# Performance work log

Measured on AMD Instinct MI355X. Metric: run time of the kernel, lower is better.

## Reference

```python
import jax, jax.numpy as jnp
import numpy as np
from jax import lax

E = 300   # word embedding dim (hard-coded embedding_size in DMCNN)
P = 5     # position-feature dim
H = 200   # conv out channels
S = 256   # max_seq_len
L = 34    # num_labels
VOCAB = 21128


def setup_inputs() -> dict:
    key = jax.random.key(0)
    ks = jax.random.split(key, 7)
    B = 8
    return {
        "inputs": jax.random.randint(ks[0], (B, S), 0, VOCAB, dtype=jnp.int64),
        "word_emb": jax.random.normal(ks[1], (VOCAB, E), dtype=jnp.float32) * 0.02,
        "pf_emb": jax.random.normal(ks[2], (S, P), dtype=jnp.float32) * 0.02,
        "conv_W": jax.random.normal(ks[3], (H, E + P, 3), dtype=jnp.float32) * 0.02,
        "conv_b": jax.random.normal(ks[4], (H,), dtype=jnp.float32) * 0.02,
        "fc_W": jax.random.normal(ks[5], (L, 3 * E + 2 * H), dtype=jnp.float32) * 0.02,
        "fc_b": jax.random.normal(ks[6], (L,), dtype=jnp.float32) * 0.02,
    }


def _conv1d(x_ncs, w_oik):
    # x: [N, C, S], w: [O, I, K], stride 1, padding 1 (kernel 3)
    return lax.conv_general_dilated(
        x_ncs, w_oik, window_strides=(1,), padding=[(1, 1)],
        dimension_numbers=("NCH", "OIH", "NCH"))


def reference(inputs, word_emb, pf_emb, conv_W, conv_b, fc_W, fc_b):
    B = inputs.shape[0]
    tok = word_emb[inputs]                       # [B, S, E]

    # Positions i = 1 .. S-2 (the original loop), fully vectorized.
    i_vals = jnp.arange(1, S - 1)                # [S-2]
    j = jnp.arange(S)
    pos_idx = jnp.abs(j[None, :] - i_vals[:, None])   # [S-2, S] == the loop's pos_index
    pf = pf_emb[pos_idx]                         # [S-2, S, P]

    # Conv is linear: split into token part (shared across i) + pf part (per i).
    W_tok, W_pf = conv_W[:, :E, :], conv_W[:, E:, :]
    conv_tok = _conv1d(tok.transpose(0, 2, 1), W_tok) + conv_b[None, :, None]  # [B, H, S]
    conv_pf = _conv1d(pf.transpose(0, 2, 1), W_pf)                             # [S-2, H, S] (batch-independent)

    out = jax.nn.relu(conv_tok[None] + conv_pf[:, None])   # [S-2, B, H, S]

    # Dynamic split max-pool at index i.
    left_mask = (j[None, :] < i_vals[:, None])[:, None, None, :]  # [S-2,1,1,S]
    neg_inf = jnp.array(-jnp.inf, dtype=out.dtype)
    max_left = jnp.where(left_mask, out, neg_inf).max(axis=-1)    # [S-2, B, H]
    max_right = jnp.where(left_mask, neg_inf, out).max(axis=-1)   # [S-2, B, H]
    pool = jnp.concatenate([max_left, max_right], axis=-1)        # [S-2, B, 2H]

    # Lexical-level features: window [i-1, i, i+1] flattened.
    llf = jnp.concatenate([tok[:, 0:S - 2], tok[:, 1:S - 1], tok[:, 2:S]], axis=-1)  # [B, S-2, 3E]

    feat = jnp.concatenate([pool.transpose(1, 0, 2), llf], axis=-1)  # [B, S-2, 2H+3E]
    logits_mid = jnp.einsum("bsf,lf->bsl", feat, fc_W) + fc_b        # [B, S-2, L]

    pad = jnp.zeros((B, 1, L), dtype=logits_mid.dtype).at[:, :, -1].set(1.0)
    return jnp.concatenate([pad, logits_mid, pad], axis=1)          # [B, S, L]
```

## Files before the change

kernel.cpp:

```cpp
#include <hip/hip_runtime.h>

#define E 300
#define P 5
#define H 200
#define S 256
#define L 34
#define B 8
#define NI 254

typedef __attribute__((ext_vector_type(8))) short short8;
typedef __attribute__((ext_vector_type(4))) float f32x4;

#define TOKB_OFF   0
#define TOKB_FL    309632
#define WR3_OFF    (TOKB_OFF+TOKB_FL)
#define WR3_FL     96512
#define FCWB_OFF   (WR3_OFF+WR3_FL)
#define FCWB_FL    32256
#define G_OFF      (FCWB_OFF+FCWB_FL)
#define G_FL       102400
#define C0_OFF     (G_OFF+G_FL)
#define C0_FL      50800
#define C255_OFF   (C0_OFF+C0_FL)
#define C255_FL    50800
#define CT_OFF     (C255_OFF+C255_FL)
#define CT_FL      409600
#define POOLBF_OFF (CT_OFF+CT_FL)
#define POOLBF_FL  425984

__device__ __forceinline__ unsigned short f2bf(float f) {
    unsigned u = __float_as_uint(f);
    unsigned r = (u + 0x7FFFu + ((u >> 16) & 1u)) >> 16;
    return (unsigned short)r;
}
__device__ __forceinline__ short8 load_a8(const unsigned short* p) {
    short8 r;
    ((ushort4*)&r)[0] = *(const ushort4*)p;
    ((ushort4*)&r)[1] = *(const ushort4*)(p + 4);
    return r;
}
__device__ __forceinline__ float4 add4(float4 a, float4 b) {
    return make_float4(a.x+b.x, a.y+b.y, a.z+b.z, a.w+b.w);
}
__device__ __forceinline__ float4 max4(float4 a, float4 b) {
    return make_float4(fmaxf(a.x,b.x), fmaxf(a.y,b.y), fmaxf(a.z,b.z), fmaxf(a.w,b.w));
}

#define GA_BLOCKS 605
#define PREP_BLOCKS 1803

__global__ __launch_bounds__(256) void k_init(const int* __restrict__ ids,
                                              const float* __restrict__ we,
                                              const float* __restrict__ convW,
                                              const float* __restrict__ fcW,
                                              const float* __restrict__ pf,
                                              unsigned short* __restrict__ tokb,
                                              unsigned short* __restrict__ Wr3,
                                              unsigned short* __restrict__ fcWb,
                                              float* __restrict__ g,
                                              float* __restrict__ c0,
                                              float* __restrict__ c255) {
    if (blockIdx.x < GA_BLOCKS) {
        int idx = blockIdx.x * 256 + threadIdx.x;
        const int total = B * 258 * 75;
        if (idx >= total) return;
        int row = idx / 75;
        int col = idx - row * 75;
        int b = row / 258;
        int r = row - b * 258;
        float4 v = make_float4(0.f, 0.f, 0.f, 0.f);
        if (r >= 1 && r <= 256) {
            int id = ids[b * S + (r - 1)];
            v = ((const float4*)we)[(size_t)id * 75 + col];
        }
        ushort4 o;
        o.x = f2bf(v.x); o.y = f2bf(v.y); o.z = f2bf(v.z); o.w = f2bf(v.w);
        *(ushort4*)(tokb + (size_t)row * 300 + col * 4) = o;
        return;
    }
    int idx = (blockIdx.x - GA_BLOCKS) * 256 + threadIdx.x;
    if (idx < 193024) {
        int hh = idx / 928, kk = idx - hh * 928;
        float v = 0.f;
        if (hh < H && kk < 900) {
            int r = kk / 300, e = kk - r * 300;
            v = convW[hh * 915 + e * 3 + r];
        }
        Wr3[idx] = f2bf(v);
    } else if (idx < 257536) {
        int t = idx - 193024;
        int l = t / 1344, c = t - l * 1344;
        float v = 0.f;
        if (l < L) {
            if (c < 400) v = fcW[l * 1300 + c];
            else if (c >= 416 && c < 1316) v = fcW[l * 1300 + 400 + (c - 416)];
        }
        fcWb[t] = f2bf(v);
    } else if (idx < 359936) {
        int t = idx - 257536;
        int t2 = t / H, h = t - t2 * H;
        int d = t2 - 256;
        float a = 0.f;
#pragma unroll
        for (int k = 0; k < 3; k++) {
            int r = d + k - 1; r = (r < 0) ? -r : r; if (r > 255) r = 255;
#pragma unroll
            for (int q = 0; q < P; q++)
                a += convW[h * 915 + (E + q) * 3 + k] * pf[r * P + q];
        }
        g[t] = a;
    } else if (idx < 410736) {
        int t = idx - 359936;
        int m = t / H, h = t - m * H;
        int i = m + 1;
        float a = 0.f;
#pragma unroll
        for (int q = 0; q < P; q++) {
            a += convW[h * 915 + (E + q) * 3 + 1] * pf[i * P + q];
            a += convW[h * 915 + (E + q) * 3 + 2] * pf[(i - 1) * P + q];
        }
        c0[m * H + h] = a;
    } else if (idx < 461536) {
        int t = idx - 410736;
        int m = t / H, h = t - m * H;
        int i = m + 1;
        float a = 0.f;
#pragma unroll
        for (int q = 0; q < P; q++) {
            a += convW[h * 915 + (E + q) * 3 + 0] * pf[(254 - i) * P + q];
            a += convW[h * 915 + (E + q) * 3 + 1] * pf[(255 - i) * P + q];
        }
        c255[m * H + h] = a;
    }
}

__global__ __launch_bounds__(256) void k_conv(const unsigned short* __restrict__ tokb,
                                              const unsigned short* __restrict__ Wr3,
                                              const float* __restrict__ convB,
                                              float* __restrict__ ct) {
    int n0 = blockIdx.x * 16;
    int mg = blockIdx.y;
    int wave = threadIdx.x >> 6;
    int lane = threadIdx.x & 63;
    int quad = lane >> 4;
    int lr = lane & 15;
    int mtile = mg * 4 + wave;
    int b = mtile >> 4;
    int j0 = (mtile & 15) << 4;

    const unsigned short* pa = tokb + ((size_t)(b * 258 + j0 + lr) * 300 + quad * 8);
    const unsigned short* pb = Wr3 + ((size_t)(n0 + lr) * 928 + quad * 8);

    f32x4 acc0 = {0.f, 0.f, 0.f, 0.f};
    f32x4 acc1 = {0.f, 0.f, 0.f, 0.f};
#pragma unroll
    for (int kk = 0; kk + 1 < 29; kk += 2) {
        short8 a0 = load_a8(pa + kk * 32);
        short8 b0 = *(const short8*)(pb + kk * 32);
        acc0 = __builtin_amdgcn_mfma_f32_16x16x32_bf16(a0, b0, acc0, 0, 0, 0);
        short8 a1 = load_a8(pa + kk * 32 + 32);
        short8 b1 = *(const short8*)(pb + kk * 32 + 32);
        acc1 = __builtin_amdgcn_mfma_f32_16x16x32_bf16(a1, b1, acc1, 0, 0, 0);
    }
    {
        short8 a0 = load_a8(pa + 28 * 32);
        short8 b0 = *(const short8*)(pb + 28 * 32);
        acc0 = __builtin_amdgcn_mfma_f32_16x16x32_bf16(a0, b0, acc0, 0, 0, 0);
    }
    int h = n0 + lr;
    if (h < H) {
        float bias = convB[h];
        float* cp = ct + ((size_t)(b * 256 + j0 + quad * 4) * 200 + h);
#pragma unroll
        for (int r = 0; r < 4; r++)
            cp[(size_t)r * 200] = acc0[r] + acc1[r] + bias;
    }
}

__global__ __launch_bounds__(512) void k_poolA(const float* __restrict__ ct,
                                               const float* __restrict__ g,
                                               const float* __restrict__ c0,
                                               const float* __restrict__ c255,
                                               unsigned short* __restrict__ poolbf) {
    __shared__ float4 lds4[8 * 4 * 2 * 50];
    int pg = blockIdx.x;
    int b  = blockIdx.y;
    int tid = threadIdx.x;
    int sub = tid >> 6;
    int lane = tid & 63;
    int p0 = pg * 4 + 1;

    if (lane < 50) {
        int h = lane << 2;
        const float* ctb = ct + (size_t)b * S * H + h;
        const float* gb  = g + h;

        float4 aL0 = {0,0,0,0}, aL1 = aL0, aL2 = aL0, aL3 = aL0;
        float4 aR0 = aL0, aR1 = aL0, aR2 = aL0, aR3 = aL0;

        if (sub == 0) {
            float4 c = *(const float4*)(ctb);
            int m = pg * 4;
            if (m + 0 < NI) aL0 = max4(aL0, add4(c, *(const float4*)(c0 + (m+0) * H + h)));
            if (m + 1 < NI) aL1 = max4(aL1, add4(c, *(const float4*)(c0 + (m+1) * H + h)));
            if (m + 2 < NI) aL2 = max4(aL2, add4(c, *(const float4*)(c0 + (m+2) * H + h)));
            if (m + 3 < NI) aL3 = max4(aL3, add4(c, *(const float4*)(c0 + (m+3) * H + h)));
        }
        if (sub == 7) {
            float4 c = *(const float4*)(ctb + (size_t)255 * H);
            int m = pg * 4;
            if (m + 0 < NI) aR0 = max4(aR0, add4(c, *(const float4*)(c255 + (m+0) * H + h)));
            if (m + 1 < NI) aR1 = max4(aR1, add4(c, *(const float4*)(c255 + (m+1) * H + h)));
            if (m + 2 < NI) aR2 = max4(aR2, add4(c, *(const float4*)(c255 + (m+2) * H + h)));
            if (m + 3 < NI) aR3 = max4(aR3, add4(c, *(const float4*)(c255 + (m+3) * H + h)));
        }

        int js = (sub == 0) ? 1 : sub * 32;
        int je = (sub == 7) ? 254 : sub * 32 + 31;

        float4 gr0 = *(const float4*)(gb + (size_t)(js - p0 + 256) * H);
        float4 gr1 = *(const float4*)(gb + (size_t)(js - p0 + 255) * H);
        float4 gr2 = *(const float4*)(gb + (size_t)(js - p0 + 254) * H);
        float4 gr3 = *(const float4*)(gb + (size_t)(js - p0 + 253) * H);

#pragma unroll 4
        for (int j = js; j <= je; ++j) {
            float4 c = *(const float4*)(ctb + (size_t)j * H);
            float4 v0 = add4(c, gr0);
            float4 v1 = add4(c, gr1);
            float4 v2 = add4(c, gr2);
            float4 v3 = add4(c, gr3);
            if (j < p0)     aL0 = max4(aL0, v0); else aR0 = max4(aR0, v0);
            if (j < p0 + 1) aL1 = max4(aL1, v1); else aR1 = max4(aR1, v1);
            if (j < p0 + 2) aL2 = max4(aL2, v2); else aR2 = max4(aR2, v2);
            if (j < p0 + 3) aL3 = max4(aL3, v3); else aR3 = max4(aR3, v3);
            gr3 = gr2; gr2 = gr1; gr1 = gr0;
            gr0 = *(const float4*)(gb + (size_t)(j + 1 - p0 + 256) * H);
        }

        float4* lp = lds4 + (size_t)sub * 400 + lane;
        lp[0]   = aL0; lp[50]  = aR0;
        lp[100] = aL1; lp[150] = aR1;
        lp[200] = aL2; lp[250] = aR2;
        lp[300] = aL3; lp[350] = aR3;
    }
    __syncthreads();

    if (tid < 400) {
        int k = tid / 100;
        int r = tid - k * 100;
        int half = r / 50;
        int ln = r - half * 50;
        int slot = (k * 2 + half) * 50 + ln;
        float4 v = lds4[slot];
#pragma unroll
        for (int s2 = 1; s2 < 8; s2++) v = max4(v, lds4[s2 * 400 + slot]);
        int m = pg * 4 + k;
        if (m < NI) {
            ushort4 o;
            o.x = f2bf(v.x); o.y = f2bf(v.y); o.z = f2bf(v.z); o.w = f2bf(v.w);
            *(ushort4*)(poolbf + (size_t)(b * 256 + m + 1) * 416 + half * 200 + ln * 4) = o;
        }
    } else if (tid < 464) {
        int t = tid - 400;
        int k = t >> 4, c = t & 15;
        int m = pg * 4 + k;
        if (m < NI) poolbf[(size_t)(b * 256 + m + 1) * 416 + 400 + c] = 0;
    }
}

__global__ __launch_bounds__(256) void k_fc(const unsigned short* __restrict__ poolbf,
                                            const unsigned short* __restrict__ tokb,
                                            const unsigned short* __restrict__ fcWb,
                                            const float* __restrict__ fcB,
                                            float* __restrict__ out) {
    int n0 = blockIdx.x * 16;
    int mg = blockIdx.y;
    int wave = threadIdx.x >> 6;
    int lane = threadIdx.x & 63;
    int quad = lane >> 4;
    int lr = lane & 15;
    int mtile = mg * 4 + wave;
    int b = mtile >> 4;
    int s0 = (mtile & 15) << 4;

    const unsigned short* pa0 = poolbf + ((size_t)(b * 256 + s0 + lr) * 416 + quad * 8);
    const unsigned short* pa1 = tokb + ((size_t)(b * 258 + s0 + lr) * 300 + quad * 8);
    const unsigned short* pb0 = fcWb + ((size_t)(n0 + lr) * 1344 + quad * 8);
    const unsigned short* pb1 = pb0 + 416;

    f32x4 acc0 = {0.f, 0.f, 0.f, 0.f};
    f32x4 acc1 = {0.f, 0.f, 0.f, 0.f};
    int kk = 0;
#pragma unroll 3
    for (kk = 0; kk + 1 < 13; kk += 2) {
        short8 a0 = load_a8(pa0 + kk * 32);
        short8 b0 = *(const short8*)(pb0 + kk * 32);
        acc0 = __builtin_amdgcn_mfma_f32_16x16x32_bf16(a0, b0, acc0, 0, 0, 0);
        short8 a1 = load_a8(pa0 + kk * 32 + 32);
        short8 b1 = *(const short8*)(pb0 + kk * 32 + 32);
        acc1 = __builtin_amdgcn_mfma_f32_16x16x32_bf16(a1, b1, acc1, 0, 0, 0);
    }
    {
        short8 a0 = load_a8(pa0 + 12 * 32);
        short8 b0 = *(const short8*)(pb0 + 12 * 32);
        acc0 = __builtin_amdgcn_mfma_f32_16x16x32_bf16(a0, b0, acc0, 0, 0, 0);
    }
#pragma unroll 4
    for (kk = 0; kk + 1 < 29; kk += 2) {
        short8 a0 = load_a8(pa1 + kk * 32);
        short8 b0 = *(const short8*)(pb1 + kk * 32);
        acc0 = __builtin_amdgcn_mfma_f32_16x16x32_bf16(a0, b0, acc0, 0, 0, 0);
        short8 a1 = load_a8(pa1 + kk * 32 + 32);
        short8 b1 = *(const short8*)(pb1 + kk * 32 + 32);
        acc1 = __builtin_amdgcn_mfma_f32_16x16x32_bf16(a1, b1, acc1, 0, 0, 0);
    }
    {
        short8 a0 = load_a8(pa1 + 28 * 32);
        short8 b0 = *(const short8*)(pb1 + 28 * 32);
        acc0 = __builtin_amdgcn_mfma_f32_16x16x32_bf16(a0, b0, acc0, 0, 0, 0);
    }

    int l = n0 + lr;
    if (l < L) {
        float bias = fcB[l];
#pragma unroll
        for (int r = 0; r < 4; r++) {
            int s = s0 + quad * 4 + r;
            float val;
            if (s == 0 || s == S - 1) val = (l == L - 1) ? 1.0f : 0.0f;
            else                      val = acc0[r] + acc1[r] + bias;
            out[(size_t)(b * 256 + s) * L + l] = val;
        }
    }
}

extern "C" void kernel_launch(void* const* d_in, const int* in_sizes, int n_in,
                              void* d_out, int out_size, void* d_ws, size_t ws_size,
                              hipStream_t stream) {
    const int*   ids      = (const int*)d_in[0];
    const float* word_emb = (const float*)d_in[1];
    const float* pf_emb   = (const float*)d_in[2];
    const float* conv_W   = (const float*)d_in[3];
    const float* conv_b   = (const float*)d_in[4];
    const float* fc_W     = (const float*)d_in[5];
    const float* fc_b     = (const float*)d_in[6];
    float* out = (float*)d_out;
    float* ws  = (float*)d_ws;

    unsigned short* tokb   = (unsigned short*)(ws + TOKB_OFF);
    unsigned short* Wr3    = (unsigned short*)(ws + WR3_OFF);
    unsigned short* fcWb   = (unsigned short*)(ws + FCWB_OFF);
    float* g     = ws + G_OFF;
    float* c0    = ws + C0_OFF;
    float* c255  = ws + C255_OFF;
    float* ct    = ws + CT_OFF;
    unsigned short* poolbf = (unsigned short*)(ws + POOLBF_OFF);

    k_init<<<GA_BLOCKS + PREP_BLOCKS, 256, 0, stream>>>(ids, word_emb, conv_W, fc_W,
                                                        pf_emb, tokb, Wr3, fcWb,
                                                        g, c0, c255);
    k_conv<<<dim3(13, 32), 256, 0, stream>>>(tokb, Wr3, conv_b, ct);
    k_poolA<<<dim3(64, 8), 512, 0, stream>>>(ct, g, c0, c255, poolbf);
    k_fc<<<dim3(3, 32), 256, 0, stream>>>(poolbf, tokb, fcWb, fc_b, out);
}
```

Before: 133.7 us.

## Store conv intermediates in bf16 and split pool loop into branch-free ranges

The conv output ct and the positional tables g, c0 and c255 are now stored as bf16 instead of fp32, which halves the bytes the pooling kernel reads from memory. The pooling j-loop is split into a pure-left range, a short mixed range of four iterations and a pure-right range, so the per-element left/right branch disappears from most iterations. The pool kernel also gets a min-blocks launch bound. The cost is lower precision in intermediates that feed a max, which could move outputs past tolerance.

```diff
diff --git a/kernel.cpp b/kernel.cpp
--- a/kernel.cpp
+++ b/kernel.cpp
@@ -13,25 +13,31 @@
 
 #define TOKB_OFF   0
 #define TOKB_FL    309632
-#define WR3_OFF    (TOKB_OFF+TOKB_FL)
+#define WR3_OFF    309632
 #define WR3_FL     96512
-#define FCWB_OFF   (WR3_OFF+WR3_FL)
+#define FCWB_OFF   406144
 #define FCWB_FL    32256
-#define G_OFF      (FCWB_OFF+FCWB_FL)
-#define G_FL       102400
-#define C0_OFF     (G_OFF+G_FL)
-#define C0_FL      50800
-#define C255_OFF   (C0_OFF+C0_FL)
-#define C255_FL    50800
-#define CT_OFF     (C255_OFF+C255_FL)
-#define CT_FL      409600
-#define POOLBF_OFF (CT_OFF+CT_FL)
+#define G_OFF      438400
+#define G_FL       51200
+#define C0_OFF     489600
+#define C0_FL      25400
+#define C255_OFF   515000
+#define C255_FL    25400
+#define CT_OFF     540400
+#define CT_FL      204800
+#define POOLBF_OFF 745200
 #define POOLBF_FL  425984
 
 __device__ __forceinline__ unsigned short f2bf(float f) {
     unsigned u = __float_as_uint(f);
     unsigned r = (u + 0x7FFFu + ((u >> 16) & 1u)) >> 16;
     return (unsigned short)r;
+}
+__device__ __forceinline__ float bfu(unsigned short s) {
+    return __uint_as_float(((unsigned)s) << 16);
+}
+__device__ __forceinline__ float4 bf4(ushort4 u) {
+    return make_float4(bfu(u.x), bfu(u.y), bfu(u.z), bfu(u.w));
 }
 __device__ __forceinline__ short8 load_a8(const unsigned short* p) {
     short8 r;
@@ -57,9 +63,9 @@
                                               unsigned short* __restrict__ tokb,
                                               unsigned short* __restrict__ Wr3,
                                               unsigned short* __restrict__ fcWb,
-                                              float* __restrict__ g,
-                                              float* __restrict__ c0,
-                                              float* __restrict__ c255) {
+                                              unsigned short* __restrict__ g,
+                                              unsigned short* __restrict__ c0,
+                                              unsigned short* __restrict__ c255) {
     if (blockIdx.x < GA_BLOCKS) {
         int idx = blockIdx.x * 256 + threadIdx.x;
         const int total = B * 258 * 75;
@@ -108,7 +114,7 @@
             for (int q = 0; q < P; q++)
                 a += convW[h * 915 + (E + q) * 3 + k] * pf[r * P + q];
         }
-        g[t] = a;
+        g[t] = f2bf(a);
     } else if (idx < 410736) {
         int t = idx - 359936;
         int m = t / H, h = t - m * H;
@@ -119,7 +125,7 @@
             a += convW[h * 915 + (E + q) * 3 + 1] * pf[i * P + q];
             a += convW[h * 915 + (E + q) * 3 + 2] * pf[(i - 1) * P + q];
         }
-        c0[m * H + h] = a;
+        c0[m * H + h] = f2bf(a);
     } else if (idx < 461536) {
         int t = idx - 410736;
         int m = t / H, h = t - m * H;
@@ -130,14 +136,14 @@
             a += convW[h * 915 + (E + q) * 3 + 0] * pf[(254 - i) * P + q];
             a += convW[h * 915 + (E + q) * 3 + 1] * pf[(255 - i) * P + q];
         }
-        c255[m * H + h] = a;
+        c255[m * H + h] = f2bf(a);
     }
 }
 
 __global__ __launch_bounds__(256) void k_conv(const unsigned short* __restrict__ tokb,
                                               const unsigned short* __restrict__ Wr3,
                                               const float* __restrict__ convB,
-                                              float* __restrict__ ct) {
+                                              unsigned short* __restrict__ ct) {
     int n0 = blockIdx.x * 16;
     int mg = blockIdx.y;
     int wave = threadIdx.x >> 6;
@@ -170,18 +176,17 @@
     int h = n0 + lr;
     if (h < H) {
         float bias = convB[h];
-        float* cp = ct + ((size_t)(b * 256 + j0 + quad * 4) * 200 + h);
 #pragma unroll
         for (int r = 0; r < 4; r++)
-            cp[(size_t)r * 200] = acc0[r] + acc1[r] + bias;
-    }
-}
-
-__global__ __launch_bounds__(512) void k_poolA(const float* __restrict__ ct,
-                                               const float* __restrict__ g,
-                                               const float* __restrict__ c0,
-                                               const float* __restrict__ c255,
-                                               unsigned short* __restrict__ poolbf) {
+            ct[(size_t)(b * 256 + j0 + quad * 4 + r) * 200 + h] = f2bf(acc0[r] + acc1[r] + bias);
+    }
+}
+
+__global__ __launch_bounds__(512, 4) void k_poolA(const unsigned short* __restrict__ ct,
+                                                  const unsigned short* __restrict__ g,
+                                                  const unsigned short* __restrict__ c0,
+                                                  const unsigned short* __restrict__ c255,
+                                                  unsigned short* __restrict__ poolbf) {
     __shared__ float4 lds4[8 * 4 * 2 * 50];
     int pg = blockIdx.x;
     int b  = blockIdx.y;
@@ -192,40 +197,54 @@
 
     if (lane < 50) {
         int h = lane << 2;
-        const float* ctb = ct + (size_t)b * S * H + h;
-        const float* gb  = g + h;
+        const unsigned short* ctb = ct + (size_t)b * S * H + h;
+        const unsigned short* gb  = g + h;
 
         float4 aL0 = {0,0,0,0}, aL1 = aL0, aL2 = aL0, aL3 = aL0;
         float4 aR0 = aL0, aR1 = aL0, aR2 = aL0, aR3 = aL0;
 
         if (sub == 0) {
-            float4 c = *(const float4*)(ctb);
+            float4 c = bf4(*(const ushort4*)(ctb));
             int m = pg * 4;
-            if (m + 0 < NI) aL0 = max4(aL0, add4(c, *(const float4*)(c0 + (m+0) * H + h)));
-            if (m + 1 < NI) aL1 = max4(aL1, add4(c, *(const float4*)(c0 + (m+1) * H + h)));
-            if (m + 2 < NI) aL2 = max4(aL2, add4(c, *(const float4*)(c0 + (m+2) * H + h)));
-            if (m + 3 < NI) aL3 = max4(aL3, add4(c, *(const float4*)(c0 + (m+3) * H + h)));
+            if (m + 0 < NI) aL0 = max4(aL0, add4(c, bf4(*(const ushort4*)(c0 + (m+0) * H + h))));
+            if (m + 1 < NI) aL1 = max4(aL1, add4(c, bf4(*(const ushort4*)(c0 + (m+1) * H + h))));
+            if (m + 2 < NI) aL2 = max4(aL2, add4(c, bf4(*(const ushort4*)(c0 + (m+2) * H + h))));
+            if (m + 3 < NI) aL3 = max4(aL3, add4(c, bf4(*(const ushort4*)(c0 + (m+3) * H + h))));
         }
         if (sub == 7) {
-            float4 c = *(const float4*)(ctb + (size_t)255 * H);
+            float4 c = bf4(*(const ushort4*)(ctb + (size_t)255 * H));
             int m = pg * 4;
-            if (m + 0 < NI) aR0 = max4(aR0, add4(c, *(const float4*)(c255 + (m+0) * H + h)));
-            if (m + 1 < NI) aR1 = max4(aR1, add4(c, *(const float4*)(c255 + (m+1) * H + h)));
-            if (m + 2 < NI) aR2 = max4(aR2, add4(c, *(const float4*)(c255 + (m+2) * H + h)));
-            if (m + 3 < NI) aR3 = max4(aR3, add4(c, *(const float4*)(c255 + (m+3) * H + h)));
+            if (m + 0 < NI) aR0 = max4(aR0, add4(c, bf4(*(const ushort4*)(c255 + (m+0) * H + h))));
+            if (m + 1 < NI) aR1 = max4(aR1, add4(c, bf4(*(const ushort4*)(c255 + (m+1) * H + h))));
+            if (m + 2 < NI) aR2 = max4(aR2, add4(c, bf4(*(const ushort4*)(c255 + (m+2) * H + h))));
+            if (m + 3 < NI) aR3 = max4(aR3, add4(c, bf4(*(const ushort4*)(c255 + (m+3) * H + h))));
         }
 
         int js = (sub == 0) ? 1 : sub * 32;
         int je = (sub == 7) ? 254 : sub * 32 + 31;
 
-        float4 gr0 = *(const float4*)(gb + (size_t)(js - p0 + 256) * H);
-        float4 gr1 = *(const float4*)(gb + (size_t)(js - p0 + 255) * H);
-        float4 gr2 = *(const float4*)(gb + (size_t)(js - p0 + 254) * H);
-        float4 gr3 = *(const float4*)(gb + (size_t)(js - p0 + 253) * H);
-
-#pragma unroll 4
-        for (int j = js; j <= je; ++j) {
-            float4 c = *(const float4*)(ctb + (size_t)j * H);
+        float4 gr0 = bf4(*(const ushort4*)(gb + (size_t)(js - p0 + 256) * H));
+        float4 gr1 = bf4(*(const ushort4*)(gb + (size_t)(js - p0 + 255) * H));
+        float4 gr2 = bf4(*(const ushort4*)(gb + (size_t)(js - p0 + 254) * H));
+        float4 gr3 = bf4(*(const ushort4*)(gb + (size_t)(js - p0 + 253) * H));
+
+        int eL = (je + 1 < p0) ? (je + 1) : p0;
+        int mS = (js > p0) ? js : p0;
+        int eM = (je + 1 < p0 + 4) ? (je + 1) : (p0 + 4);
+        int rS = (js > p0 + 4) ? js : (p0 + 4);
+
+#pragma unroll 8
+        for (int j = js; j < eL; ++j) {
+            float4 c = bf4(*(const ushort4*)(ctb + (size_t)j * H));
+            aL0 = max4(aL0, add4(c, gr0));
+            aL1 = max4(aL1, add4(c, gr1));
+            aL2 = max4(aL2, add4(c, gr2));
+            aL3 = max4(aL3, add4(c, gr3));
+            gr3 = gr2; gr2 = gr1; gr1 = gr0;
+            gr0 = bf4(*(const ushort4*)(gb + (size_t)(j + 1 - p0 + 256) * H));
+        }
+        for (int j = mS; j < eM; ++j) {
+            float4 c = bf4(*(const ushort4*)(ctb + (size_t)j * H));
             float4 v0 = add4(c, gr0);
             float4 v1 = add4(c, gr1);
             float4 v2 = add4(c, gr2);
@@ -235,7 +254,17 @@
             if (j < p0 + 2) aL2 = max4(aL2, v2); else aR2 = max4(aR2, v2);
             if (j < p0 + 3) aL3 = max4(aL3, v3); else aR3 = max4(aR3, v3);
             gr3 = gr2; gr2 = gr1; gr1 = gr0;
-            gr0 = *(const float4*)(gb + (size_t)(j + 1 - p0 + 256) * H);
+            gr0 = bf4(*(const ushort4*)(gb + (size_t)(j + 1 - p0 + 256) * H));
+        }
+#pragma unroll 8
+        for (int j = rS; j <= je; ++j) {
+            float4 c = bf4(*(const ushort4*)(ctb + (size_t)j * H));
+            aR0 = max4(aR0, add4(c, gr0));
+            aR1 = max4(aR1, add4(c, gr1));
+            aR2 = max4(aR2, add4(c, gr2));
+            aR3 = max4(aR3, add4(c, gr3));
+            gr3 = gr2; gr2 = gr1; gr1 = gr0;
+            gr0 = bf4(*(const ushort4*)(gb + (size_t)(j + 1 - p0 + 256) * H));
         }
 
         float4* lp = lds4 + (size_t)sub * 400 + lane;
@@ -351,10 +380,10 @@
     unsigned short* tokb   = (unsigned short*)(ws + TOKB_OFF);
     unsigned short* Wr3    = (unsigned short*)(ws + WR3_OFF);
     unsigned short* fcWb   = (unsigned short*)(ws + FCWB_OFF);
-    float* g     = ws + G_OFF;
-    float* c0    = ws + C0_OFF;
-    float* c255  = ws + C255_OFF;
-    float* ct    = ws + CT_OFF;
+    unsigned short* g      = (unsigned short*)(ws + G_OFF);
+    unsigned short* c0     = (unsigned short*)(ws + C0_OFF);
+    unsigned short* c255   = (unsigned short*)(ws + C255_OFF);
+    unsigned short* ct     = (unsigned short*)(ws + CT_OFF);
     unsigned short* poolbf = (unsigned short*)(ws + POOLBF_OFF);
 
     k_init<<<GA_BLOCKS + PREP_BLOCKS, 256, 0, stream>>>(ids, word_emb, conv_W, fc_W,
```

After: 352.1 us. 2.63x slower.
